# Optimization experiments

Hardware: AMD Instinct MI355X
Metric: run time of the kernel (lower is better)

## Reference

```python
import jax, jax.numpy as jnp
import numpy as np

NUM_EXPERTS = 8
TOP_K = 2
HIDDEN = 1024
INTER = 4096
LB_WEIGHT = 0.01


def setup_inputs() -> dict:
    key = jax.random.key(0)
    ks = jax.random.split(key, 6)
    s = 0.02
    return {
        "hidden_states": jax.random.normal(ks[0], (2, 2048, HIDDEN), dtype=jnp.float32),
        "Wg": jax.random.normal(ks[1], (HIDDEN, NUM_EXPERTS), dtype=jnp.float32) * s,
        "w1": jax.random.normal(ks[2], (NUM_EXPERTS, HIDDEN, INTER), dtype=jnp.float32) * s,
        "b1": jnp.zeros((NUM_EXPERTS, INTER), dtype=jnp.float32),
        "w2": jax.random.normal(ks[3], (NUM_EXPERTS, INTER, HIDDEN), dtype=jnp.float32) * s,
        "b2": jnp.zeros((NUM_EXPERTS, HIDDEN), dtype=jnp.float32),
    }


def reference(hidden_states, Wg, w1, b1, w2, b2):
    B, S, H = hidden_states.shape
    x = hidden_states.reshape(-1, H)            # [T, H]
    T = x.shape[0]

    # 1. Gating: softmax over experts, top-k selection, renormalized gates
    probs = jax.nn.softmax(x @ Wg, axis=-1)     # [T, E]
    top_v, top_i = jax.lax.top_k(probs, TOP_K)  # [T, K]
    gate = top_v / jnp.sum(top_v, axis=-1, keepdims=True)

    # Load-balancing aux loss: E * sum(frac_assigned * mean_prob) * weight
    frac = jnp.mean(jax.nn.one_hot(top_i, NUM_EXPERTS, dtype=probs.dtype), axis=(0, 1))  # [E]
    mean_p = jnp.mean(probs, axis=0)            # [E]
    aux_loss = NUM_EXPERTS * jnp.sum(frac * mean_p) * LB_WEIGHT

    # Combine weights: per-token weight for each expert (sum of matching top-k gates)
    combine = jnp.zeros((T, NUM_EXPERTS), dtype=x.dtype)
    combine = combine.at[jnp.arange(T)[:, None], top_i].add(gate)  # [T, E]

    # 2-4. Expert FFN + weighted combine (math-equivalent dense-per-expert form)
    out = jnp.zeros_like(x)
    for e in range(NUM_EXPERTS):
        h = jax.nn.gelu(x @ w1[e] + b1[e])       # [T, INTER]
        out = out + combine[:, e:e + 1] * (h @ w2[e] + b2[e])
    return out.reshape(B, S, H), aux_loss
```

## Files before the change

kernel.cpp:

```cpp
#include <hip/hip_runtime.h>
#include <hip/hip_bf16.h>

#define T_TOK   4096
#define HID     1024
#define INTER   4096
#define NEXP    8
#define MAXT    72
#define MAXSLOT 9216
#define TPB_TOK 16

typedef __attribute__((ext_vector_type(8))) short s16x8;
typedef __attribute__((ext_vector_type(4))) float f32x4;

__device__ __forceinline__ void load_lds16(const void* g, void* l) {
    __builtin_amdgcn_global_load_lds(
        (const __attribute__((address_space(1))) void*)g,
        (__attribute__((address_space(3))) void*)l, 16, 0, 0);
}

__device__ __forceinline__ float gelu_tanh(float v) {
    float c = 0.7978845608028654f;
    float z = c * (v + 0.044715f * v * v * v);
    return v / (1.0f + __expf(-2.0f * z));
}

__global__ void transpose_bf16_kernel(const float* __restrict__ in, __hip_bfloat16* __restrict__ out,
                                      int R, int C) {
    __shared__ float tile[64][65];
    size_t eoff = (size_t)blockIdx.z * R * C;
    int c0 = blockIdx.x * 64, r0 = blockIdx.y * 64;
    int tid = threadIdx.x;

    int lr = tid >> 4;
    int lc = (tid & 15) * 4;
    #pragma unroll
    for (int it = 0; it < 4; ++it) {
        int r = it * 16 + lr;
        float4 v = *(const float4*)(in + eoff + (size_t)(r0 + r) * C + c0 + lc);
        tile[r][lc + 0] = v.x; tile[r][lc + 1] = v.y;
        tile[r][lc + 2] = v.z; tile[r][lc + 3] = v.w;
    }
    __syncthreads();

    int oc = tid >> 3;
    int r8 = (tid & 7) * 8;
    #pragma unroll
    for (int it = 0; it < 2; ++it) {
        int c = it * 32 + oc;
        alignas(16) __hip_bfloat16 o[8];
        #pragma unroll
        for (int j = 0; j < 8; ++j) o[j] = __float2bfloat16(tile[r8 + j][c]);
        *(s16x8*)(out + eoff + (size_t)(c0 + c) * R + r0 + r8) = *(const s16x8*)o;
    }
}

__global__ void gating_kernel(const float* __restrict__ x, const float* __restrict__ Wg,
                              __hip_bfloat16* __restrict__ xb,
                              float* __restrict__ combine, int* __restrict__ counts,
                              float* __restrict__ prob_sums, int* __restrict__ idxcap) {
    __shared__ float s_ps[NEXP];
    __shared__ int   s_cnt[NEXP];
    __shared__ int   s_base[NEXP];
    __shared__ int   s_ei[TPB_TOK][2];
    __shared__ int   s_rk[TPB_TOK][2];

    int tid = threadIdx.x, wv = tid >> 6, ln = tid & 63;
    if (tid < NEXP) { s_ps[tid] = 0.f; s_cnt[tid] = 0; }
    __syncthreads();

    int t0 = blockIdx.x * TPB_TOK;
    for (int sub = 0; sub < 4; ++sub) {
        int tl = wv * 4 + sub;
        int t = t0 + tl;
        const float* xr = x + (size_t)t * HID + ln * 16;
        float4 xv[4];
        #pragma unroll
        for (int i = 0; i < 4; ++i) xv[i] = *(const float4*)(xr + i * 4);

        alignas(16) __hip_bfloat16 row[16];
        #pragma unroll
        for (int i = 0; i < 4; ++i) {
            row[i * 4 + 0] = __float2bfloat16(xv[i].x);
            row[i * 4 + 1] = __float2bfloat16(xv[i].y);
            row[i * 4 + 2] = __float2bfloat16(xv[i].z);
            row[i * 4 + 3] = __float2bfloat16(xv[i].w);
        }
        __hip_bfloat16* xbr = xb + (size_t)t * HID + ln * 16;
        *(s16x8*)(xbr)     = *(s16x8*)&row[0];
        *(s16x8*)(xbr + 8) = *(s16x8*)&row[8];

        float acc[NEXP] = {0,0,0,0,0,0,0,0};
        #pragma unroll
        for (int i = 0; i < 4; ++i) {
            float xs[4] = {xv[i].x, xv[i].y, xv[i].z, xv[i].w};
            #pragma unroll
            for (int j = 0; j < 4; ++j) {
                int k = ln * 16 + i * 4 + j;
                float4 wa = *(const float4*)(Wg + (size_t)k * 8);
                float4 wb = *(const float4*)(Wg + (size_t)k * 8 + 4);
                acc[0] += xs[j] * wa.x; acc[1] += xs[j] * wa.y;
                acc[2] += xs[j] * wa.z; acc[3] += xs[j] * wa.w;
                acc[4] += xs[j] * wb.x; acc[5] += xs[j] * wb.y;
                acc[6] += xs[j] * wb.z; acc[7] += xs[j] * wb.w;
            }
        }
        #pragma unroll
        for (int e = 0; e < NEXP; ++e)
            #pragma unroll
            for (int off = 32; off >= 1; off >>= 1)
                acc[e] += __shfl_xor(acc[e], off);

        float m = acc[0];
        #pragma unroll
        for (int e = 1; e < NEXP; ++e) m = fmaxf(m, acc[e]);
        float p[NEXP], s = 0.f;
        #pragma unroll
        for (int e = 0; e < NEXP; ++e) { p[e] = __expf(acc[e] - m); s += p[e]; }
        float inv = 1.0f / s;
        #pragma unroll
        for (int e = 0; e < NEXP; ++e) p[e] *= inv;

        int i0 = 0;
        #pragma unroll
        for (int e = 1; e < NEXP; ++e) if (p[e] > p[i0]) i0 = e;
        int i1 = (i0 == 0) ? 1 : 0;
        #pragma unroll
        for (int e = 0; e < NEXP; ++e) if (e != i0 && p[e] > p[i1]) i1 = e;
        float gs = p[i0] + p[i1];
        float g0 = p[i0] / gs, g1 = p[i1] / gs;

        if (ln == 0) {
            float rowc[NEXP] = {0,0,0,0,0,0,0,0};
            rowc[i0] = g0; rowc[i1] = g1;
            float4* cr = (float4*)(combine + (size_t)t * NEXP);
            cr[0] = make_float4(rowc[0], rowc[1], rowc[2], rowc[3]);
            cr[1] = make_float4(rowc[4], rowc[5], rowc[6], rowc[7]);
            #pragma unroll
            for (int e = 0; e < NEXP; ++e) atomicAdd(&s_ps[e], p[e]);
            int r0 = atomicAdd(&s_cnt[i0], 1);
            int r1 = atomicAdd(&s_cnt[i1], 1);
            s_ei[tl][0] = i0; s_rk[tl][0] = r0;
            s_ei[tl][1] = i1; s_rk[tl][1] = r1;
        }
    }
    __syncthreads();
    if (tid < NEXP) {
        s_base[tid] = atomicAdd(&counts[tid], s_cnt[tid]);
        atomicAdd(&prob_sums[tid], s_ps[tid]);
    }
    __syncthreads();
    if (tid < TPB_TOK * 2) {
        int tl = tid >> 1, k = tid & 1;
        int e = s_ei[tl][k];
        idxcap[e * T_TOK + s_base[e] + s_rk[tl][k]] = t0 + tl;
    }
}

__global__ void plan_kernel(const int* __restrict__ counts, const float* __restrict__ prob_sums,
                            int* __restrict__ offs, int* __restrict__ tile_e,
                            int* __restrict__ tile_s0, int* __restrict__ tile_nv,
                            int* __restrict__ ntiles, float* __restrict__ aux_out) {
    int tt = 0, o = 0;
    for (int e = 0; e < NEXP; ++e) {
        offs[e] = o;
        int n = counts[e];
        int nt = (n + 127) >> 7;
        for (int r = 0; r < nt; ++r) {
            tile_e[tt] = e;
            tile_s0[tt] = o + r * 128;
            int nv = n - r * 128; if (nv > 128) nv = 128;
            tile_nv[tt] = nv;
            ++tt;
        }
        o += nt * 128;
    }
    *ntiles = tt;
    float aux = 0.f;
    for (int e = 0; e < NEXP; ++e)
        aux += ((float)counts[e] / (float)(T_TOK * 2)) * (prob_sums[e] / (float)T_TOK);
    aux_out[0] = (float)NEXP * aux * 0.01f;
}

__global__ void compact_kernel(const int* __restrict__ counts, const int* __restrict__ offs,
                               const int* __restrict__ tile_e, const int* __restrict__ tile_s0,
                               const int* __restrict__ ntiles,
                               const int* __restrict__ idxcap, int* __restrict__ idxc) {
    int tt = blockIdx.x;
    if (tt >= *ntiles) return;
    int e = tile_e[tt];
    int slot = tile_s0[tt] + threadIdx.x;
    int i = slot - offs[e];
    int n = counts[e];
    idxc[slot] = (i < n) ? idxcap[e * T_TOK + i] : 0;
}


__global__ __launch_bounds__(256, 3)
void gemm1_kernel(const __hip_bfloat16* __restrict__ xb,
                  const __hip_bfloat16* __restrict__ w1b,
                  const float* __restrict__ b1,
                  const int* __restrict__ idxc,
                  const int* __restrict__ tile_e, const int* __restrict__ tile_s0,
                  const int* __restrict__ ntiles,
                  __hip_bfloat16* __restrict__ h)
{
    const int NWG = MAXT * (INTER / 128);
    int bid = blockIdx.x;
    int w = (bid & 7) * (NWG / 8) + (bid >> 3);
    int tt = w >> 5;
    int n0 = (w & 31) * 128;
    if (tt >= *ntiles) return;
    int e = tile_e[tt];
    int slot0 = tile_s0[tt];

    __shared__ __hip_bfloat16 As[128][64];
    __shared__ __hip_bfloat16 Bs[128][64];
    __shared__ int s_idx[128];

    int tid = threadIdx.x, wv = tid >> 6, ln = tid & 63;
    if (tid < 128) s_idx[tid] = idxc[slot0 + tid];
    __syncthreads();

    int swz = ((ln & 7) ^ (ln >> 3)) * 8;
    const __hip_bfloat16* srcA[4];
    const __hip_bfloat16* srcB[4];
    const __hip_bfloat16* wbase = w1b + (size_t)e * INTER * HID;
    #pragma unroll
    for (int j = 0; j < 4; ++j) {
        int r = wv * 32 + j * 8 + (ln >> 3);
        srcA[j] = xb + (size_t)s_idx[r] * HID + swz;
        srcB[j] = wbase + (size_t)(n0 + r) * HID + swz;
    }

    f32x4 acc[4][4] = {};
    int wr = wv >> 1, wc = wv & 1, lr = ln & 15;

    for (int kt = 0; kt < HID; kt += 64) {
        #pragma unroll
        for (int j = 0; j < 4; ++j) {
            load_lds16(srcA[j] + kt, (void*)&As[wv * 32 + j * 8][0]);
            load_lds16(srcB[j] + kt, (void*)&Bs[wv * 32 + j * 8][0]);
        }
        __syncthreads();
        #pragma unroll
        for (int kk = 0; kk < 2; ++kk) {
            int lslot = (((kk * 4) + (ln >> 4)) ^ (ln & 7)) * 16;
            s16x8 af[4], bf[4];
            #pragma unroll
            for (int m = 0; m < 4; ++m) {
                int row = wr * 64 + m * 16 + lr;
                af[m] = *(const s16x8*)((const char*)&As[0][0] + row * 128 + lslot);
            }
            #pragma unroll
            for (int n = 0; n < 4; ++n) {
                int row = wc * 64 + n * 16 + lr;
                bf[n] = *(const s16x8*)((const char*)&Bs[0][0] + row * 128 + lslot);
            }
            #pragma unroll
            for (int m = 0; m < 4; ++m)
                #pragma unroll
                for (int n = 0; n < 4; ++n)
                    acc[m][n] = __builtin_amdgcn_mfma_f32_16x16x32_bf16(af[m], bf[n], acc[m][n], 0, 0, 0);
        }
        __syncthreads();
    }

    const float* b1e = b1 + (size_t)e * INTER;
    int rq = (ln >> 4) * 4;
    #pragma unroll
    for (int m = 0; m < 4; ++m) {
        #pragma unroll
        for (int r = 0; r < 4; ++r) {
            int row = wr * 64 + m * 16 + rq + r;
            size_t hrow = (size_t)(slot0 + row) * INTER;
            #pragma unroll
            for (int n = 0; n < 4; ++n) {
                int col = n0 + wc * 64 + n * 16 + lr;
                float v = acc[m][n][r] + b1e[col];
                h[hrow + col] = __float2bfloat16(gelu_tanh(v));
            }
        }
    }
}

__global__ __launch_bounds__(256, 3)
void gemm2_kernel(const __hip_bfloat16* __restrict__ h,
                  const __hip_bfloat16* __restrict__ w2b,
                  const float* __restrict__ b2,
                  const float* __restrict__ combine,
                  const int* __restrict__ idxc,
                  const int* __restrict__ tile_e, const int* __restrict__ tile_s0,
                  const int* __restrict__ tile_nv, const int* __restrict__ ntiles,
                  float* __restrict__ out)
{
    const int NWG = MAXT * (HID / 128) * 2;
    int bid = blockIdx.x;
    int w = (bid & 7) * (NWG / 8) + (bid >> 3);
    int ks = w & 1;
    int n0 = ((w >> 1) & 7) * 128;
    int tt = w >> 4;
    if (tt >= *ntiles) return;
    int e = tile_e[tt];
    int slot0 = tile_s0[tt];

    __shared__ __hip_bfloat16 As[128][64];
    __shared__ __hip_bfloat16 Bs[128][64];
    __shared__ int s_idx[128];

    int tid = threadIdx.x, wv = tid >> 6, ln = tid & 63;
    if (tid < 128) s_idx[tid] = idxc[slot0 + tid];
    __syncthreads();

    int swz = ((ln & 7) ^ (ln >> 3)) * 8;
    const __hip_bfloat16* srcA[4];
    const __hip_bfloat16* srcB[4];
    const __hip_bfloat16* wbase = w2b + (size_t)e * HID * INTER;
    #pragma unroll
    for (int j = 0; j < 4; ++j) {
        int r = wv * 32 + j * 8 + (ln >> 3);
        srcA[j] = h + (size_t)(slot0 + r) * INTER + swz;
        srcB[j] = wbase + (size_t)(n0 + r) * INTER + swz;
    }

    f32x4 acc[4][4] = {};
    int wr = wv >> 1, wc = wv & 1, lr = ln & 15;

    int k0 = ks * (INTER / 2), k1 = k0 + INTER / 2;
    for (int kt = k0; kt < k1; kt += 64) {
        #pragma unroll
        for (int j = 0; j < 4; ++j) {
            load_lds16(srcA[j] + kt, (void*)&As[wv * 32 + j * 8][0]);
            load_lds16(srcB[j] + kt, (void*)&Bs[wv * 32 + j * 8][0]);
        }
        __syncthreads();
        #pragma unroll
        for (int kk = 0; kk < 2; ++kk) {
            int lslot = (((kk * 4) + (ln >> 4)) ^ (ln & 7)) * 16;
            s16x8 af[4], bf[4];
            #pragma unroll
            for (int m = 0; m < 4; ++m) {
                int row = wr * 64 + m * 16 + lr;
                af[m] = *(const s16x8*)((const char*)&As[0][0] + row * 128 + lslot);
            }
            #pragma unroll
            for (int n = 0; n < 4; ++n) {
                int row = wc * 64 + n * 16 + lr;
                bf[n] = *(const s16x8*)((const char*)&Bs[0][0] + row * 128 + lslot);
            }
            #pragma unroll
            for (int m = 0; m < 4; ++m)
                #pragma unroll
                for (int n = 0; n < 4; ++n)
                    acc[m][n] = __builtin_amdgcn_mfma_f32_16x16x32_bf16(af[m], bf[n], acc[m][n], 0, 0, 0);
        }
        __syncthreads();
    }

    const float* b2e = b2 + (size_t)e * HID;
    int nv = tile_nv[tt];
    int rq = (ln >> 4) * 4;
    #pragma unroll
    for (int m = 0; m < 4; ++m) {
        #pragma unroll
        for (int r = 0; r < 4; ++r) {
            int row = wr * 64 + m * 16 + rq + r;
            if (row < nv) {
                int tok = s_idx[row];
                float g = combine[(size_t)tok * 8 + e];
                #pragma unroll
                for (int n = 0; n < 4; ++n) {
                    int col = n0 + wc * 64 + n * 16 + lr;
                    float v = acc[m][n][r] + (ks == 0 ? b2e[col] : 0.f);
                    atomicAdd(&out[(size_t)tok * HID + col], g * v);
                }
            }
        }
    }
}

static const size_t OFF_XB      = 0;
static const size_t SZ_XB       = (size_t)T_TOK * HID * 2;
static const size_t OFF_W1B     = OFF_XB + SZ_XB;
static const size_t SZ_W        = (size_t)NEXP * INTER * HID * 2;
static const size_t OFF_W2B     = OFF_W1B + SZ_W;
static const size_t OFF_H       = OFF_W2B + SZ_W;
static const size_t SZ_H        = (size_t)MAXSLOT * INTER * 2;
static const size_t OFF_COMBINE = OFF_H + SZ_H;
static const size_t OFF_IDXCAP  = OFF_COMBINE + (size_t)T_TOK * 8 * 4;
static const size_t OFF_IDXC    = OFF_IDXCAP + (size_t)NEXP * T_TOK * 4;
static const size_t OFF_COUNTS  = OFF_IDXC + (size_t)MAXSLOT * 4;
static const size_t OFF_PSUMS   = OFF_COUNTS + 32;
static const size_t OFF_OFFS    = OFF_PSUMS + 32;
static const size_t OFF_TILE_E  = OFF_OFFS + 64;
static const size_t OFF_TILE_S0 = OFF_TILE_E + 512;
static const size_t OFF_TILE_NV = OFF_TILE_S0 + 512;
static const size_t OFF_NTILES  = OFF_TILE_NV + 512;

extern "C" void kernel_launch(void* const* d_in, const int* in_sizes, int n_in,
                              void* d_out, int out_size, void* d_ws, size_t ws_size,
                              hipStream_t stream) {
    const float* x  = (const float*)d_in[0];
    const float* Wg = (const float*)d_in[1];
    const float* w1 = (const float*)d_in[2];
    const float* b1 = (const float*)d_in[3];
    const float* w2 = (const float*)d_in[4];
    const float* b2 = (const float*)d_in[5];
    float* out = (float*)d_out;
    char* ws = (char*)d_ws;

    __hip_bfloat16* xb   = (__hip_bfloat16*)(ws + OFF_XB);
    __hip_bfloat16* w1b  = (__hip_bfloat16*)(ws + OFF_W1B);
    __hip_bfloat16* w2b  = (__hip_bfloat16*)(ws + OFF_W2B);
    __hip_bfloat16* h    = (__hip_bfloat16*)(ws + OFF_H);
    float* combine       = (float*)(ws + OFF_COMBINE);
    int*   idxcap        = (int*)(ws + OFF_IDXCAP);
    int*   idxc          = (int*)(ws + OFF_IDXC);
    int*   counts        = (int*)(ws + OFF_COUNTS);
    float* psums         = (float*)(ws + OFF_PSUMS);
    int*   offs          = (int*)(ws + OFF_OFFS);
    int*   tile_e        = (int*)(ws + OFF_TILE_E);
    int*   tile_s0       = (int*)(ws + OFF_TILE_S0);
    int*   tile_nv       = (int*)(ws + OFF_TILE_NV);
    int*   ntiles        = (int*)(ws + OFF_NTILES);

    (void)hipMemsetAsync(out, 0, (size_t)out_size * sizeof(float), stream);
    (void)hipMemsetAsync(ws + OFF_COUNTS, 0, 64, stream);

    transpose_bf16_kernel<<<dim3(INTER / 64, HID / 64, NEXP), 256, 0, stream>>>(w1, w1b, HID, INTER);
    transpose_bf16_kernel<<<dim3(HID / 64, INTER / 64, NEXP), 256, 0, stream>>>(w2, w2b, INTER, HID);
    gating_kernel<<<T_TOK / TPB_TOK, 256, 0, stream>>>(x, Wg, xb, combine, counts, psums, idxcap);
    plan_kernel<<<1, 1, 0, stream>>>(counts, psums, offs, tile_e, tile_s0, tile_nv, ntiles,
                                     out + (size_t)T_TOK * HID);
    compact_kernel<<<MAXT, 128, 0, stream>>>(counts, offs, tile_e, tile_s0, ntiles, idxcap, idxc);
    gemm1_kernel<<<MAXT * (INTER / 128), 256, 0, stream>>>(xb, w1b, b1, idxc, tile_e, tile_s0,
                                                           ntiles, h);
    gemm2_kernel<<<MAXT * (HID / 128) * 2, 256, 0, stream>>>(h, w2b, b2, combine, idxc, tile_e,
                                                             tile_s0, tile_nv, ntiles, out);
}
```

Baseline: 370.2 us.

## Double-buffer LDS tiles with BK=32 in both expert GEMM kernels

Both expert GEMM kernels now use two LDS buffers of 128x32 bf16 instead of a single 128x64 buffer. The next K-slice's global-to-LDS load is issued before computing on the current one, so there is one barrier per iteration instead of two. Precomputed 32-bit offsets replace 64-bit pointers, and a new XOR swizzle matches the narrower rows. This hides load latency behind MFMA work, at the cost of twice as many loop iterations and a 4-way swizzle that may bank-conflict more.

```diff
diff --git a/kernel.cpp b/kernel.cpp
--- a/kernel.cpp
+++ b/kernel.cpp
@@ -213,57 +213,62 @@
     int e = tile_e[tt];
     int slot0 = tile_s0[tt];
 
-    __shared__ __hip_bfloat16 As[128][64];
-    __shared__ __hip_bfloat16 Bs[128][64];
+    __shared__ __hip_bfloat16 As[2][128][32];
+    __shared__ __hip_bfloat16 Bs[2][128][32];
     __shared__ int s_idx[128];
 
     int tid = threadIdx.x, wv = tid >> 6, ln = tid & 63;
     if (tid < 128) s_idx[tid] = idxc[slot0 + tid];
     __syncthreads();
 
-    int swz = ((ln & 7) ^ (ln >> 3)) * 8;
-    const __hip_bfloat16* srcA[4];
-    const __hip_bfloat16* srcB[4];
-    const __hip_bfloat16* wbase = w1b + (size_t)e * INTER * HID;
-    #pragma unroll
-    for (int j = 0; j < 4; ++j) {
-        int r = wv * 32 + j * 8 + (ln >> 3);
-        srcA[j] = xb + (size_t)s_idx[r] * HID + swz;
-        srcB[j] = wbase + (size_t)(n0 + r) * HID + swz;
+    int sg = ((ln & 3) ^ ((ln >> 3) & 3)) * 8;
+    unsigned offA[2], offB[2];
+    #pragma unroll
+    for (int j = 0; j < 2; ++j) {
+        int r = wv * 32 + j * 16 + (ln >> 2);
+        offA[j] = (unsigned)(s_idx[r] * HID + sg);
+        offB[j] = (unsigned)(((unsigned)(e * INTER + n0 + r)) * HID + sg);
     }
 
     f32x4 acc[4][4] = {};
     int wr = wv >> 1, wc = wv & 1, lr = ln & 15;
-
-    for (int kt = 0; kt < HID; kt += 64) {
-        #pragma unroll
-        for (int j = 0; j < 4; ++j) {
-            load_lds16(srcA[j] + kt, (void*)&As[wv * 32 + j * 8][0]);
-            load_lds16(srcB[j] + kt, (void*)&Bs[wv * 32 + j * 8][0]);
-        }
+    int pA = ((ln >> 4) ^ ((lr >> 1) & 3)) * 16;
+
+    auto STAGE = [&](int b, int kt) {
+        #pragma unroll
+        for (int j = 0; j < 2; ++j) {
+            load_lds16(xb  + offA[j] + kt, (void*)&As[b][wv * 32 + j * 16][0]);
+            load_lds16(w1b + offB[j] + kt, (void*)&Bs[b][wv * 32 + j * 16][0]);
+        }
+    };
+    auto COMPUTE = [&](int b) {
+        s16x8 af[4], bf[4];
+        #pragma unroll
+        for (int m = 0; m < 4; ++m) {
+            int row = wr * 64 + m * 16 + lr;
+            af[m] = *(const s16x8*)((const char*)&As[b][0][0] + row * 64 + pA);
+        }
+        #pragma unroll
+        for (int n = 0; n < 4; ++n) {
+            int row = wc * 64 + n * 16 + lr;
+            bf[n] = *(const s16x8*)((const char*)&Bs[b][0][0] + row * 64 + pA);
+        }
+        #pragma unroll
+        for (int m = 0; m < 4; ++m)
+            #pragma unroll
+            for (int n = 0; n < 4; ++n)
+                acc[m][n] = __builtin_amdgcn_mfma_f32_16x16x32_bf16(af[m], bf[n], acc[m][n], 0, 0, 0);
+    };
+
+    STAGE(0, 0);
+    __syncthreads();
+    const int NT = HID / 32;
+    for (int t = 0; t < NT - 1; ++t) {
+        STAGE((t + 1) & 1, (t + 1) * 32);
+        COMPUTE(t & 1);
         __syncthreads();
-        #pragma unroll
-        for (int kk = 0; kk < 2; ++kk) {
-            int lslot = (((kk * 4) + (ln >> 4)) ^ (ln & 7)) * 16;
-            s16x8 af[4], bf[4];
-            #pragma unroll
-            for (int m = 0; m < 4; ++m) {
-                int row = wr * 64 + m * 16 + lr;
-                af[m] = *(const s16x8*)((const char*)&As[0][0] + row * 128 + lslot);
-            }
-            #pragma unroll
-            for (int n = 0; n < 4; ++n) {
-                int row = wc * 64 + n * 16 + lr;
-                bf[n] = *(const s16x8*)((const char*)&Bs[0][0] + row * 128 + lslot);
-            }
-            #pragma unroll
-            for (int m = 0; m < 4; ++m)
-                #pragma unroll
-                for (int n = 0; n < 4; ++n)
-                    acc[m][n] = __builtin_amdgcn_mfma_f32_16x16x32_bf16(af[m], bf[n], acc[m][n], 0, 0, 0);
-        }
-        __syncthreads();
-    }
+    }
+    COMPUTE((NT - 1) & 1);
 
     const float* b1e = b1 + (size_t)e * INTER;
     int rq = (ln >> 4) * 4;
@@ -303,58 +308,63 @@
     int e = tile_e[tt];
     int slot0 = tile_s0[tt];
 
-    __shared__ __hip_bfloat16 As[128][64];
-    __shared__ __hip_bfloat16 Bs[128][64];
+    __shared__ __hip_bfloat16 As[2][128][32];
+    __shared__ __hip_bfloat16 Bs[2][128][32];
     __shared__ int s_idx[128];
 
     int tid = threadIdx.x, wv = tid >> 6, ln = tid & 63;
     if (tid < 128) s_idx[tid] = idxc[slot0 + tid];
     __syncthreads();
 
-    int swz = ((ln & 7) ^ (ln >> 3)) * 8;
-    const __hip_bfloat16* srcA[4];
-    const __hip_bfloat16* srcB[4];
-    const __hip_bfloat16* wbase = w2b + (size_t)e * HID * INTER;
-    #pragma unroll
-    for (int j = 0; j < 4; ++j) {
-        int r = wv * 32 + j * 8 + (ln >> 3);
-        srcA[j] = h + (size_t)(slot0 + r) * INTER + swz;
-        srcB[j] = wbase + (size_t)(n0 + r) * INTER + swz;
+    int sg = ((ln & 3) ^ ((ln >> 3) & 3)) * 8;
+    unsigned offA[2], offB[2];
+    #pragma unroll
+    for (int j = 0; j < 2; ++j) {
+        int r = wv * 32 + j * 16 + (ln >> 2);
+        offA[j] = (unsigned)((unsigned)(slot0 + r) * INTER + sg);
+        offB[j] = (unsigned)(((unsigned)(e * HID + n0 + r)) * INTER + sg);
     }
 
     f32x4 acc[4][4] = {};
     int wr = wv >> 1, wc = wv & 1, lr = ln & 15;
-
-    int k0 = ks * (INTER / 2), k1 = k0 + INTER / 2;
-    for (int kt = k0; kt < k1; kt += 64) {
-        #pragma unroll
-        for (int j = 0; j < 4; ++j) {
-            load_lds16(srcA[j] + kt, (void*)&As[wv * 32 + j * 8][0]);
-            load_lds16(srcB[j] + kt, (void*)&Bs[wv * 32 + j * 8][0]);
-        }
+    int pA = ((ln >> 4) ^ ((lr >> 1) & 3)) * 16;
+
+    auto STAGE = [&](int b, int kt) {
+        #pragma unroll
+        for (int j = 0; j < 2; ++j) {
+            load_lds16(h   + offA[j] + kt, (void*)&As[b][wv * 32 + j * 16][0]);
+            load_lds16(w2b + offB[j] + kt, (void*)&Bs[b][wv * 32 + j * 16][0]);
+        }
+    };
+    auto COMPUTE = [&](int b) {
+        s16x8 af[4], bf[4];
+        #pragma unroll
+        for (int m = 0; m < 4; ++m) {
+            int row = wr * 64 + m * 16 + lr;
+            af[m] = *(const s16x8*)((const char*)&As[b][0][0] + row * 64 + pA);
+        }
+        #pragma unroll
+        for (int n = 0; n < 4; ++n) {
+            int row = wc * 64 + n * 16 + lr;
+            bf[n] = *(const s16x8*)((const char*)&Bs[b][0][0] + row * 64 + pA);
+        }
+        #pragma unroll
+        for (int m = 0; m < 4; ++m)
+            #pragma unroll
+            for (int n = 0; n < 4; ++n)
+                acc[m][n] = __builtin_amdgcn_mfma_f32_16x16x32_bf16(af[m], bf[n], acc[m][n], 0, 0, 0);
+    };
+
+    int k0 = ks * (INTER / 2);
+    STAGE(0, k0);
+    __syncthreads();
+    const int NT = (INTER / 2) / 32;
+    for (int t = 0; t < NT - 1; ++t) {
+        STAGE((t + 1) & 1, k0 + (t + 1) * 32);
+        COMPUTE(t & 1);
         __syncthreads();
-        #pragma unroll
-        for (int kk = 0; kk < 2; ++kk) {
-            int lslot = (((kk * 4) + (ln >> 4)) ^ (ln & 7)) * 16;
-            s16x8 af[4], bf[4];
-            #pragma unroll
-            for (int m = 0; m < 4; ++m) {
-                int row = wr * 64 + m * 16 + lr;
-                af[m] = *(const s16x8*)((const char*)&As[0][0] + row * 128 + lslot);
-            }
-            #pragma unroll
-            for (int n = 0; n < 4; ++n) {
-                int row = wc * 64 + n * 16 + lr;
-                bf[n] = *(const s16x8*)((const char*)&Bs[0][0] + row * 128 + lslot);
-            }
-            #pragma unroll
-            for (int m = 0; m < 4; ++m)
-                #pragma unroll
-                for (int n = 0; n < 4; ++n)
-                    acc[m][n] = __builtin_amdgcn_mfma_f32_16x16x32_bf16(af[m], bf[n], acc[m][n], 0, 0, 0);
-        }
-        __syncthreads();
-    }
+    }
+    COMPUTE((NT - 1) & 1);
 
     const float* b2e = b2 + (size_t)e * HID;
     int nv = tile_nv[tt];
```

After: 402.6 us. 8.7% more time.

## Shrink expert row tiles to 64 tokens with two-wave workgroups

Applied to the files above, without the earlier changes.

Expert token tiles drop from 128 to 64 rows, so per-expert padding waste shrinks and there are more tiles. Both GEMMs now run 128-thread workgroups with a 64x128 output tile, each wave covering 64 columns. Load addressing switches to 32-bit offsets. The cost is that each weight tile is reused across fewer tokens, raising weight traffic per FLOP, and LDS per block gets smaller.

```diff
diff --git a/kernel.cpp b/kernel.cpp
--- a/kernel.cpp
+++ b/kernel.cpp
@@ -5,8 +5,8 @@
 #define HID     1024
 #define INTER   4096
 #define NEXP    8
-#define MAXT    72
-#define MAXSLOT 9216
+#define MAXT64  136
+#define MSLOT64 8704
 #define TPB_TOK 16
 
 typedef __attribute__((ext_vector_type(8))) short s16x8;
@@ -164,15 +164,15 @@
     for (int e = 0; e < NEXP; ++e) {
         offs[e] = o;
         int n = counts[e];
-        int nt = (n + 127) >> 7;
+        int nt = (n + 63) >> 6;
         for (int r = 0; r < nt; ++r) {
             tile_e[tt] = e;
-            tile_s0[tt] = o + r * 128;
-            int nv = n - r * 128; if (nv > 128) nv = 128;
+            tile_s0[tt] = o + r * 64;
+            int nv = n - r * 64; if (nv > 64) nv = 64;
             tile_nv[tt] = nv;
             ++tt;
         }
-        o += nt * 128;
+        o += nt * 64;
     }
     *ntiles = tt;
     float aux = 0.f;
@@ -195,7 +195,7 @@
 }
 
 
-__global__ __launch_bounds__(256, 3)
+__global__ __launch_bounds__(128, 3)
 void gemm1_kernel(const __hip_bfloat16* __restrict__ xb,
                   const __hip_bfloat16* __restrict__ w1b,
                   const float* __restrict__ b1,
@@ -204,7 +204,7 @@
                   const int* __restrict__ ntiles,
                   __hip_bfloat16* __restrict__ h)
 {
-    const int NWG = MAXT * (INTER / 128);
+    const int NWG = MAXT64 * (INTER / 128);
     int bid = blockIdx.x;
     int w = (bid & 7) * (NWG / 8) + (bid >> 3);
     int tt = w >> 5;
@@ -213,34 +213,31 @@
     int e = tile_e[tt];
     int slot0 = tile_s0[tt];
 
-    __shared__ __hip_bfloat16 As[128][64];
+    __shared__ __hip_bfloat16 As[64][64];
     __shared__ __hip_bfloat16 Bs[128][64];
-    __shared__ int s_idx[128];
-
-    int tid = threadIdx.x, wv = tid >> 6, ln = tid & 63;
-    if (tid < 128) s_idx[tid] = idxc[slot0 + tid];
-    __syncthreads();
-
-    int swz = ((ln & 7) ^ (ln >> 3)) * 8;
-    const __hip_bfloat16* srcA[4];
-    const __hip_bfloat16* srcB[4];
-    const __hip_bfloat16* wbase = w1b + (size_t)e * INTER * HID;
+    __shared__ int s_idx[64];
+
+    int tid = threadIdx.x, wid = tid >> 6, ln = tid & 63;
+    if (tid < 64) s_idx[tid] = idxc[slot0 + tid];
+    __syncthreads();
+
+    int sg = ((ln & 7) ^ ((ln >> 3) & 7)) * 8;
+    unsigned offA[4];
     #pragma unroll
-    for (int j = 0; j < 4; ++j) {
-        int r = wv * 32 + j * 8 + (ln >> 3);
-        srcA[j] = xb + (size_t)s_idx[r] * HID + swz;
-        srcB[j] = wbase + (size_t)(n0 + r) * HID + swz;
-    }
+    for (int j = 0; j < 4; ++j)
+        offA[j] = (unsigned)(s_idx[j * 16 + wid * 8 + (ln >> 3)] * HID) + sg;
+    unsigned offB0 = (unsigned)((e * INTER + n0 + wid * 8 + (ln >> 3)) * HID) + sg;
 
     f32x4 acc[4][4] = {};
-    int wr = wv >> 1, wc = wv & 1, lr = ln & 15;
+    int lr = ln & 15;
 
     for (int kt = 0; kt < HID; kt += 64) {
         #pragma unroll
-        for (int j = 0; j < 4; ++j) {
-            load_lds16(srcA[j] + kt, (void*)&As[wv * 32 + j * 8][0]);
-            load_lds16(srcB[j] + kt, (void*)&Bs[wv * 32 + j * 8][0]);
-        }
+        for (int j = 0; j < 4; ++j)
+            load_lds16(xb + offA[j] + kt, (void*)&As[j * 16 + wid * 8][0]);
+        #pragma unroll
+        for (int j = 0; j < 8; ++j)
+            load_lds16(w1b + offB0 + j * 16 * HID + kt, (void*)&Bs[j * 16 + wid * 8][0]);
         __syncthreads();
         #pragma unroll
         for (int kk = 0; kk < 2; ++kk) {
@@ -248,12 +245,12 @@
             s16x8 af[4], bf[4];
             #pragma unroll
             for (int m = 0; m < 4; ++m) {
-                int row = wr * 64 + m * 16 + lr;
+                int row = m * 16 + lr;
                 af[m] = *(const s16x8*)((const char*)&As[0][0] + row * 128 + lslot);
             }
             #pragma unroll
             for (int n = 0; n < 4; ++n) {
-                int row = wc * 64 + n * 16 + lr;
+                int row = wid * 64 + n * 16 + lr;
                 bf[n] = *(const s16x8*)((const char*)&Bs[0][0] + row * 128 + lslot);
             }
             #pragma unroll
@@ -271,11 +268,11 @@
     for (int m = 0; m < 4; ++m) {
         #pragma unroll
         for (int r = 0; r < 4; ++r) {
-            int row = wr * 64 + m * 16 + rq + r;
+            int row = m * 16 + rq + r;
             size_t hrow = (size_t)(slot0 + row) * INTER;
             #pragma unroll
             for (int n = 0; n < 4; ++n) {
-                int col = n0 + wc * 64 + n * 16 + lr;
+                int col = n0 + wid * 64 + n * 16 + lr;
                 float v = acc[m][n][r] + b1e[col];
                 h[hrow + col] = __float2bfloat16(gelu_tanh(v));
             }
@@ -283,7 +280,7 @@
     }
 }
 
-__global__ __launch_bounds__(256, 3)
+__global__ __launch_bounds__(128, 3)
 void gemm2_kernel(const __hip_bfloat16* __restrict__ h,
                   const __hip_bfloat16* __restrict__ w2b,
                   const float* __restrict__ b2,
@@ -293,7 +290,7 @@
                   const int* __restrict__ tile_nv, const int* __restrict__ ntiles,
                   float* __restrict__ out)
 {
-    const int NWG = MAXT * (HID / 128) * 2;
+    const int NWG = MAXT64 * (HID / 128) * 2;
     int bid = blockIdx.x;
     int w = (bid & 7) * (NWG / 8) + (bid >> 3);
     int ks = w & 1;
@@ -303,35 +300,29 @@
     int e = tile_e[tt];
     int slot0 = tile_s0[tt];
 
-    __shared__ __hip_bfloat16 As[128][64];
+    __shared__ __hip_bfloat16 As[64][64];
     __shared__ __hip_bfloat16 Bs[128][64];
-    __shared__ int s_idx[128];
-
-    int tid = threadIdx.x, wv = tid >> 6, ln = tid & 63;
-    if (tid < 128) s_idx[tid] = idxc[slot0 + tid];
-    __syncthreads();
-
-    int swz = ((ln & 7) ^ (ln >> 3)) * 8;
-    const __hip_bfloat16* srcA[4];
-    const __hip_bfloat16* srcB[4];
-    const __hip_bfloat16* wbase = w2b + (size_t)e * HID * INTER;
-    #pragma unroll
-    for (int j = 0; j < 4; ++j) {
-        int r = wv * 32 + j * 8 + (ln >> 3);
-        srcA[j] = h + (size_t)(slot0 + r) * INTER + swz;
-        srcB[j] = wbase + (size_t)(n0 + r) * INTER + swz;
-    }
+    __shared__ int s_idx[64];
+
+    int tid = threadIdx.x, wid = tid >> 6, ln = tid & 63;
+    if (tid < 64) s_idx[tid] = idxc[slot0 + tid];
+    __syncthreads();
+
+    int sg = ((ln & 7) ^ ((ln >> 3) & 7)) * 8;
+    unsigned offA0 = (unsigned)((slot0 + wid * 8 + (ln >> 3)) * INTER) + sg;
+    unsigned offB0 = (unsigned)((e * HID + n0 + wid * 8 + (ln >> 3)) * INTER) + sg;
 
     f32x4 acc[4][4] = {};
-    int wr = wv >> 1, wc = wv & 1, lr = ln & 15;
+    int lr = ln & 15;
 
     int k0 = ks * (INTER / 2), k1 = k0 + INTER / 2;
     for (int kt = k0; kt < k1; kt += 64) {
         #pragma unroll
-        for (int j = 0; j < 4; ++j) {
-            load_lds16(srcA[j] + kt, (void*)&As[wv * 32 + j * 8][0]);
-            load_lds16(srcB[j] + kt, (void*)&Bs[wv * 32 + j * 8][0]);
-        }
+        for (int j = 0; j < 4; ++j)
+            load_lds16(h + offA0 + j * 16 * INTER + kt, (void*)&As[j * 16 + wid * 8][0]);
+        #pragma unroll
+        for (int j = 0; j < 8; ++j)
+            load_lds16(w2b + offB0 + j * 16 * INTER + kt, (void*)&Bs[j * 16 + wid * 8][0]);
         __syncthreads();
         #pragma unroll
         for (int kk = 0; kk < 2; ++kk) {
@@ -339,12 +330,12 @@
             s16x8 af[4], bf[4];
             #pragma unroll
             for (int m = 0; m < 4; ++m) {
-                int row = wr * 64 + m * 16 + lr;
+                int row = m * 16 + lr;
                 af[m] = *(const s16x8*)((const char*)&As[0][0] + row * 128 + lslot);
             }
             #pragma unroll
             for (int n = 0; n < 4; ++n) {
-                int row = wc * 64 + n * 16 + lr;
+                int row = wid * 64 + n * 16 + lr;
                 bf[n] = *(const s16x8*)((const char*)&Bs[0][0] + row * 128 + lslot);
             }
             #pragma unroll
@@ -363,13 +354,13 @@
     for (int m = 0; m < 4; ++m) {
         #pragma unroll
         for (int r = 0; r < 4; ++r) {
-            int row = wr * 64 + m * 16 + rq + r;
+            int row = m * 16 + rq + r;
             if (row < nv) {
                 int tok = s_idx[row];
                 float g = combine[(size_t)tok * 8 + e];
                 #pragma unroll
                 for (int n = 0; n < 4; ++n) {
-                    int col = n0 + wc * 64 + n * 16 + lr;
+                    int col = n0 + wid * 64 + n * 16 + lr;
                     float v = acc[m][n][r] + (ks == 0 ? b2e[col] : 0.f);
                     atomicAdd(&out[(size_t)tok * HID + col], g * v);
                 }
@@ -384,17 +375,17 @@
 static const size_t SZ_W        = (size_t)NEXP * INTER * HID * 2;
 static const size_t OFF_W2B     = OFF_W1B + SZ_W;
 static const size_t OFF_H       = OFF_W2B + SZ_W;
-static const size_t SZ_H        = (size_t)MAXSLOT * INTER * 2;
+static const size_t SZ_H        = (size_t)MSLOT64 * INTER * 2;
 static const size_t OFF_COMBINE = OFF_H + SZ_H;
 static const size_t OFF_IDXCAP  = OFF_COMBINE + (size_t)T_TOK * 8 * 4;
 static const size_t OFF_IDXC    = OFF_IDXCAP + (size_t)NEXP * T_TOK * 4;
-static const size_t OFF_COUNTS  = OFF_IDXC + (size_t)MAXSLOT * 4;
+static const size_t OFF_COUNTS  = OFF_IDXC + (size_t)MSLOT64 * 4;
 static const size_t OFF_PSUMS   = OFF_COUNTS + 32;
 static const size_t OFF_OFFS    = OFF_PSUMS + 32;
 static const size_t OFF_TILE_E  = OFF_OFFS + 64;
-static const size_t OFF_TILE_S0 = OFF_TILE_E + 512;
-static const size_t OFF_TILE_NV = OFF_TILE_S0 + 512;
-static const size_t OFF_NTILES  = OFF_TILE_NV + 512;
+static const size_t OFF_TILE_S0 = OFF_TILE_E + 1024;
+static const size_t OFF_TILE_NV = OFF_TILE_S0 + 1024;
+static const size_t OFF_NTILES  = OFF_TILE_NV + 1024;
 
 extern "C" void kernel_launch(void* const* d_in, const int* in_sizes, int n_in,
                               void* d_out, int out_size, void* d_ws, size_t ws_size,
@@ -431,9 +422,9 @@
     gating_kernel<<<T_TOK / TPB_TOK, 256, 0, stream>>>(x, Wg, xb, combine, counts, psums, idxcap);
     plan_kernel<<<1, 1, 0, stream>>>(counts, psums, offs, tile_e, tile_s0, tile_nv, ntiles,
                                      out + (size_t)T_TOK * HID);
-    compact_kernel<<<MAXT, 128, 0, stream>>>(counts, offs, tile_e, tile_s0, ntiles, idxcap, idxc);
-    gemm1_kernel<<<MAXT * (INTER / 128), 256, 0, stream>>>(xb, w1b, b1, idxc, tile_e, tile_s0,
-                                                           ntiles, h);
-    gemm2_kernel<<<MAXT * (HID / 128) * 2, 256, 0, stream>>>(h, w2b, b2, combine, idxc, tile_e,
-                                                             tile_s0, tile_nv, ntiles, out);
-}
+    compact_kernel<<<MAXT64, 64, 0, stream>>>(counts, offs, tile_e, tile_s0, ntiles, idxcap, idxc);
+    gemm1_kernel<<<MAXT64 * (INTER / 128), 128, 0, stream>>>(xb, w1b, b1, idxc, tile_e, tile_s0,
+                                                             ntiles, h);
+    gemm2_kernel<<<MAXT64 * (HID / 128) * 2, 128, 0, stream>>>(h, w2b, b2, combine, idxc, tile_e,
+                                                               tile_s0, tile_nv, ntiles, out);
+}
```

Result: slower. 388.2 us (+4.9%).
